# Performance work log

Hardware: AMD Instinct MI355X
Metric: run time of the kernel (lower is better)

## Reference

```python
import jax, jax.numpy as jnp
import numpy as np
import math

N_HEADS = 16  # from init_kwargs

def setup_inputs() -> dict:
    key = jax.random.key(0)
    ks = jax.random.split(key, 8)
    B, S, D = 2, 2048, 1024
    dk = D // N_HEADS
    # rotary frequencies: theta_i = 10000^(-2i/dk), angles = pos * theta
    inv_freq = 1.0 / (10000.0 ** (jnp.arange(0, dk, 2, dtype=jnp.float32) / dk))
    angles = jnp.arange(S, dtype=jnp.float32)[:, None] * inv_freq[None, :]  # [S, dk/2]
    scale = 0.02
    return {
        "x": jax.random.normal(ks[0], (B, S, D), dtype=jnp.float32),
        "freq_cos": jnp.cos(angles),
        "freq_sin": jnp.sin(angles),
        "Wq": jax.random.normal(ks[1], (D, D), dtype=jnp.float32) * scale,
        "Wk": jax.random.normal(ks[2], (D, D), dtype=jnp.float32) * scale,
        "Wv": jax.random.normal(ks[3], (D, D), dtype=jnp.float32) * scale,
        "Wo": jax.random.normal(ks[4], (D, D), dtype=jnp.float32) * scale,
    }

def _apply_rope(t, freq_cos, freq_sin):
    # t: [B, S, H, dk]; interpret last dim as dk/2 complex pairs (even=real, odd=imag)
    B, S, H, dk = t.shape
    tr = t.reshape(B, S, H, dk // 2, 2)
    re, im = tr[..., 0], tr[..., 1]
    c = freq_cos[None, :, None, :]  # [1, S, 1, dk/2]
    s = freq_sin[None, :, None, :]
    out_re = re * c - im * s
    out_im = re * s + im * c
    return jnp.stack([out_re, out_im], axis=-1).reshape(B, S, H, dk)

def reference(x, freq_cos, freq_sin, Wq, Wk, Wv, Wo):
    B, S, D = x.shape
    H = N_HEADS
    dk = D // H
    q = (x @ Wq).reshape(B, S, H, dk)
    k = (x @ Wk).reshape(B, S, H, dk)
    v = (x @ Wv).reshape(B, S, H, dk)
    q = _apply_rope(q, freq_cos, freq_sin)
    k = _apply_rope(k, freq_cos, freq_sin)
    # [B, H, S, dk]
    q = q.transpose(0, 2, 1, 3)
    k = k.transpose(0, 2, 1, 3)
    v = v.transpose(0, 2, 1, 3)
    scores = jnp.einsum('bhqd,bhkd->bhqk', q, k) / math.sqrt(dk)
    # faithful to source: softmax applied TWICE
    p = jax.nn.softmax(scores, axis=-1)
    p = jax.nn.softmax(p, axis=-1)
    out = jnp.einsum('bhqk,bhkd->bhqd', p, v)
    out = out.transpose(0, 2, 1, 3).reshape(B, S, D)
    return out @ Wo
```

## Files before the change

kernel.cpp:

```cpp
#include <hip/hip_runtime.h>
#include <cstdint>

typedef unsigned short u16;
typedef unsigned int u32;
typedef __attribute__((ext_vector_type(8))) short bf16x8;
typedef __attribute__((ext_vector_type(4))) short bf16x4;
typedef __attribute__((ext_vector_type(4))) float f32x4;

__device__ __forceinline__ float bf2f(short h) {
  union { u32 u; float f; } x; x.u = ((u32)(u16)h) << 16; return x.f;
}
__device__ __forceinline__ short f2bf(float f) {
  union { float f; u32 u; } x; x.f = f;
  u32 r = x.u + 0x7fffu + ((x.u >> 16) & 1u);
  return (short)(u16)(r >> 16);
}

__device__ __forceinline__ void gload16(const void* g, void* l) {
  __builtin_amdgcn_global_load_lds(
      (const __attribute__((address_space(1))) u32*)g,
      (__attribute__((address_space(3))) u32*)l, 16, 0, 0);
}

__global__ __launch_bounds__(256) void cast_k(const float* __restrict__ in,
                                              u16* __restrict__ out) {
  int i = blockIdx.x * 256 + threadIdx.x;
  const float4* p = (const float4*)(in + (size_t)i * 8);
  float4 a = p[0], b = p[1];
  bf16x8 v;
  v[0] = f2bf(a.x); v[1] = f2bf(a.y); v[2] = f2bf(a.z); v[3] = f2bf(a.w);
  v[4] = f2bf(b.x); v[5] = f2bf(b.y); v[6] = f2bf(b.z); v[7] = f2bf(b.w);
  *(bf16x8*)(out + (size_t)i * 8) = v;
}

__global__ __launch_bounds__(256) void castT4_k(
    const float* __restrict__ W0, const float* __restrict__ W1,
    const float* __restrict__ W2, const float* __restrict__ W3,
    u16* __restrict__ O0, u16* __restrict__ O1,
    u16* __restrict__ O2, u16* __restrict__ O3) {
  __shared__ u16 Ts[64 * 72];
  const int z = blockIdx.z;
  const float* in = z == 0 ? W0 : (z == 1 ? W1 : (z == 2 ? W2 : W3));
  u16* out = z == 0 ? O0 : (z == 1 ? O1 : (z == 2 ? O2 : O3));
  const int k0 = blockIdx.x * 64, n0 = blockIdx.y * 64;
  const int t = threadIdx.x;
  const int kr = t >> 4, nc = (t & 15) * 4;
#pragma unroll
  for (int p = 0; p < 4; ++p) {
    float4 v = *(const float4*)(in + (size_t)(k0 + kr + p * 16) * 1024 + n0 + nc);
    int kk = kr + p * 16;
    Ts[(nc + 0) * 72 + kk] = (u16)f2bf(v.x);
    Ts[(nc + 1) * 72 + kk] = (u16)f2bf(v.y);
    Ts[(nc + 2) * 72 + kk] = (u16)f2bf(v.z);
    Ts[(nc + 3) * 72 + kk] = (u16)f2bf(v.w);
  }
  __syncthreads();
  const int nr = t >> 2, kc = (t & 3) * 16;
  bf16x8 o0, o1;
#pragma unroll
  for (int j = 0; j < 8; ++j) {
    o0[j] = (short)Ts[nr * 72 + kc + j];
    o1[j] = (short)Ts[nr * 72 + kc + 8 + j];
  }
  *(bf16x8*)(out + (size_t)(n0 + nr) * 1024 + k0 + kc) = o0;
  *(bf16x8*)(out + (size_t)(n0 + nr) * 1024 + k0 + kc + 8) = o1;
}

template <int OUT_BF16, int NJ>
__device__ __forceinline__ void gemm_body(char* gsm, const u16* __restrict__ A,
                                          const u16* __restrict__ Bt,
                                          void* __restrict__ Cv,
                                          int row0, int col0) {
  constexpr int SB = 16384 + NJ * 4096;
  const int t = threadIdx.x;
  const int l = t & 63, w = t >> 6;
  const int lq = l & 15, g = l >> 4;
  const int wr = w >> 1, wc = w & 1;
  const int r8 = t >> 3;
  const int c8 = (((t & 7) ^ (r8 & 7)) << 3);

  f32x4 acc[4][NJ] = {};

  auto stage = [&](int cb, int k0) {
    char* dst = gsm + cb * SB + w * 1024;
#pragma unroll
    for (int p = 0; p < 4; ++p)
      gload16(A + (size_t)(row0 + r8 + 32 * p) * 1024 + k0 + c8, dst + p * 4096);
#pragma unroll
    for (int p = 0; p < NJ; ++p)
      gload16(Bt + (size_t)(col0 + r8 + 32 * p) * 1024 + k0 + c8,
              dst + 16384 + p * 4096);
  };

  stage(0, 0);
  __syncthreads();
  int cur = 0;
  for (int k0 = 0; k0 < 1024; k0 += 64) {
    if (k0 + 64 < 1024) stage(cur ^ 1, k0 + 64);
    const char* Ab = gsm + cur * SB;
#pragma unroll
    for (int ks = 0; ks < 2; ++ks) {
      bf16x8 af[4], bfr[NJ];
      const int sA = ks * 4 + g;
#pragma unroll
      for (int i = 0; i < 4; ++i) {
        int ra = wr * 64 + i * 16 + lq;
        af[i] = *(const bf16x8*)(Ab + ra * 128 + ((sA ^ (ra & 7)) << 4));
      }
#pragma unroll
      for (int j = 0; j < NJ; ++j) {
        int rb = wc * (NJ * 16) + j * 16 + lq;
        bfr[j] = *(const bf16x8*)(Ab + 16384 + rb * 128 + ((sA ^ (rb & 7)) << 4));
      }
#pragma unroll
      for (int i = 0; i < 4; ++i)
#pragma unroll
        for (int j = 0; j < NJ; ++j)
          acc[i][j] = __builtin_amdgcn_mfma_f32_16x16x32_bf16(af[i], bfr[j],
                                                              acc[i][j], 0, 0, 0);
    }
    __syncthreads();
    cur ^= 1;
  }

#pragma unroll
  for (int i = 0; i < 4; ++i)
#pragma unroll
    for (int j = 0; j < NJ; ++j)
#pragma unroll
      for (int jr = 0; jr < 4; ++jr) {
        int row = row0 + wr * 64 + i * 16 + 4 * g + jr;
        int col = col0 + wc * (NJ * 16) + j * 16 + lq;
        float v = acc[i][j][jr];
        if (OUT_BF16)
          ((u16*)Cv)[(size_t)row * 1024 + col] = (u16)f2bf(v);
        else
          ((float*)Cv)[(size_t)row * 1024 + col] = v;
      }
}

__global__ __launch_bounds__(256) void gemm_qkv_k(
    const u16* __restrict__ xb, const u16* __restrict__ Wqt,
    const u16* __restrict__ Wkt, const u16* __restrict__ Wvt,
    u16* __restrict__ Qr, u16* __restrict__ Kr, u16* __restrict__ Vr) {
  __shared__ __align__(16) char gsm[65536];
  const int which = blockIdx.y >> 3;
  const u16* Bt = which == 0 ? Wqt : (which == 1 ? Wkt : Wvt);
  u16* C = which == 0 ? Qr : (which == 1 ? Kr : Vr);
  gemm_body<1, 4>(gsm, xb, Bt, (void*)C, blockIdx.x * 128, (blockIdx.y & 7) * 128);
}

__global__ __launch_bounds__(256) void gemm_o_k(const u16* __restrict__ A,
                                                const u16* __restrict__ Bt,
                                                float* __restrict__ C) {
  __shared__ __align__(16) char gsm[49152];
  gemm_body<0, 2>(gsm, A, Bt, (void*)C, blockIdx.x * 128, blockIdx.y * 64);
}

__global__ __launch_bounds__(256) void rope2_k(const u16* __restrict__ Qr,
                                               const u16* __restrict__ Kr,
                                               u16* __restrict__ Qb,
                                               u16* __restrict__ Kb,
                                               const float* __restrict__ cosT,
                                               const float* __restrict__ sinT) {
  const int z = blockIdx.y;
  const u16* in = z ? Kr : Qr;
  u16* out = z ? Kb : Qb;
  const float scale = z ? 1.0f : 0.18033688011112042f;
  int i = blockIdx.x * 256 + threadIdx.x;
  size_t e = (size_t)i * 8;
  int m = (int)(e >> 10), n = (int)(e & 1023);
  int b = m >> 11, s = m & 2047, h = n >> 6, d = n & 63;
  float4 c4 = *(const float4*)(cosT + s * 32 + (d >> 1));
  float4 s4 = *(const float4*)(sinT + s * 32 + (d >> 1));
  bf16x8 v = *(const bf16x8*)(in + e);
  float cc[4] = {c4.x, c4.y, c4.z, c4.w}, sn[4] = {s4.x, s4.y, s4.z, s4.w};
  bf16x8 o;
#pragma unroll
  for (int j = 0; j < 4; ++j) {
    float re = bf2f(v[2 * j]), im = bf2f(v[2 * j + 1]);
    o[2 * j] = f2bf((re * cc[j] - im * sn[j]) * scale);
    o[2 * j + 1] = f2bf((re * sn[j] + im * cc[j]) * scale);
  }
  *(bf16x8*)(out + ((size_t)((b * 16 + h) * 2048 + s)) * 64 + d) = o;
}

__global__ __launch_bounds__(256) void transV_k(const u16* __restrict__ Vr,
                                                u16* __restrict__ Vt) {
  __shared__ u16 Ls[64 * 72];
  const int bh = blockIdx.y, s0 = blockIdx.x * 64;
  const int b = bh >> 4, h = bh & 15;
  const int t = threadIdx.x;
  const int sr = t >> 3, su = t & 7;
#pragma unroll
  for (int p = 0; p < 2; ++p) {
    int srow = sr + p * 32;
    bf16x8 v = *(const bf16x8*)(Vr + (size_t)(b * 2048 + s0 + srow) * 1024 + h * 64 + su * 8);
    *(bf16x8*)((char*)Ls + (srow * 72 + su * 8) * 2) = v;
  }
  __syncthreads();
  const int d = t >> 2, sc = (t & 3) * 16;
  const int base = (sc & 32) + ((sc >> 4) & 1) * 4;
  u16* dst = Vt + ((size_t)bh * 64 + d) * 2048 + s0 + base;
#pragma unroll
  for (int q = 0; q < 4; ++q) {
    bf16x4 c;
#pragma unroll
    for (int jj = 0; jj < 4; ++jj) c[jj] = (short)Ls[(sc + q * 4 + jj) * 72 + d];
    *(bf16x4*)(dst + 8 * q) = c;
  }
}

__global__ __launch_bounds__(256) void sumv_k(const u16* __restrict__ Vr,
                                              float* __restrict__ sumVp) {
  __shared__ float Ls[32][64];
  const int h = blockIdx.x, b = blockIdx.y, sl = blockIdx.z;
  const int t = threadIdx.x;
  const int d0 = (t & 7) * 8, rg = t >> 3;
  float a[8] = {};
#pragma unroll 4
  for (int i = 0; i < 16; ++i) {
    int r = sl * 512 + rg + i * 32;
    bf16x8 v = *(const bf16x8*)(Vr + (size_t)(b * 2048 + r) * 1024 + h * 64 + d0);
#pragma unroll
    for (int j = 0; j < 8; ++j) a[j] += bf2f(v[j]);
  }
#pragma unroll
  for (int j = 0; j < 8; ++j) Ls[rg][d0 + j] = a[j];
  __syncthreads();
  if (t < 64) {
    float tot = 0.f;
#pragma unroll
    for (int r2 = 0; r2 < 32; ++r2) tot += Ls[r2][t];
    sumVp[((size_t)sl * 32 + b * 16 + h) * 64 + t] = tot;
  }
}

__global__ __launch_bounds__(256) void attn_k(const u16* __restrict__ Qb,
                                              const u16* __restrict__ Kb,
                                              const u16* __restrict__ Vt,
                                              const float* __restrict__ sumVp,
                                              u16* __restrict__ Cb) {
  __shared__ __align__(16) char smem[33280];
  float* Lbuf = (float*)(smem + 32768);
  const int t = threadIdx.x;
  const int l = t & 63, w = t >> 6;
  const int lq = l & 15, g = l >> 4;
  const int qh = w & 1, kh = w >> 1;
  const int bh = blockIdx.y, q0 = blockIdx.x * 32;
  const int b = bh >> 4, h = bh & 15;

  const u16* qrow = Qb + ((size_t)bh * 2048 + q0 + qh * 16 + lq) * 64;
  const bf16x8 qf0 = *(const bf16x8*)(qrow + g * 8);
  const bf16x8 qf1 = *(const bf16x8*)(qrow + 32 + g * 8);

  const int r8 = t >> 3;
  const int c8 = (((t & 7) ^ (r8 & 7)) << 3);
  const size_t kbase = (size_t)bh * 2048 * 64;
  const size_t vbase = (size_t)bh * 64 * 2048;

  auto stage = [&](int cb, int j0) {
    char* dst = smem + cb * 16384 + w * 1024;
#pragma unroll
    for (int p = 0; p < 2; ++p) {
      gload16(Kb + kbase + (size_t)(j0 + r8 + 32 * p) * 64 + c8, dst + p * 4096);
      gload16(Vt + vbase + (size_t)(r8 + 32 * p) * 2048 + j0 + c8,
              dst + 8192 + p * 4096);
    }
  };

  float l1 = 0.0f;
  f32x4 accO[4] = {};

  stage(0, 0);
  __syncthreads();
  int cur = 0;
  for (int j0 = 0; j0 < 2048; j0 += 64) {
    if (j0 + 64 < 2048) stage(cur ^ 1, j0 + 64);
    const char* Kl = smem + cur * 16384;
    const char* Vl = Kl + 8192;
    f32x4 sc[2] = {};
#pragma unroll
    for (int ks = 0; ks < 2; ++ks)
#pragma unroll
      for (int kt = 0; kt < 2; ++kt) {
        int r = kh * 32 + kt * 16 + lq, sA = ks * 4 + g;
        bf16x8 af = *(const bf16x8*)(Kl + r * 128 + ((sA ^ (r & 7)) << 4));
        sc[kt] = __builtin_amdgcn_mfma_f32_16x16x32_bf16(af, ks ? qf1 : qf0,
                                                         sc[kt], 0, 0, 0);
      }
    float wv[2][4];
#pragma unroll
    for (int kt = 0; kt < 2; ++kt)
#pragma unroll
      for (int jr = 0; jr < 4; ++jr) {
        float e;
        asm("v_exp_f32 %0, %1" : "=v"(e) : "v"(sc[kt][jr]));
        wv[kt][jr] = e;
        l1 += e;
      }
    union { bf16x8 v; u32 uw[4]; } pb;
    asm("v_cvt_pk_bf16_f32 %0, %1, %2" : "=v"(pb.uw[0]) : "v"(wv[0][0]), "v"(wv[0][1]));
    asm("v_cvt_pk_bf16_f32 %0, %1, %2" : "=v"(pb.uw[1]) : "v"(wv[0][2]), "v"(wv[0][3]));
    asm("v_cvt_pk_bf16_f32 %0, %1, %2" : "=v"(pb.uw[2]) : "v"(wv[1][0]), "v"(wv[1][1]));
    asm("v_cvt_pk_bf16_f32 %0, %1, %2" : "=v"(pb.uw[3]) : "v"(wv[1][2]), "v"(wv[1][3]));
#pragma unroll
    for (int dt = 0; dt < 4; ++dt) {
      int dd = dt * 16 + lq;
      bf16x8 av = *(const bf16x8*)(Vl + dd * 128 +
                                   (((kh * 4 + g) ^ (dd & 7)) << 4));
      accO[dt] = __builtin_amdgcn_mfma_f32_16x16x32_bf16(av, pb.v, accO[dt], 0, 0, 0);
    }
    __syncthreads();
    cur ^= 1;
  }

  l1 += __shfl_xor(l1, 16);
  l1 += __shfl_xor(l1, 32);
  if (l < 16) Lbuf[w * 16 + l] = l1;
  __syncthreads();
  const float l1tot = Lbuf[w * 16 + lq] + Lbuf[(w ^ 2) * 16 + lq];
  const float rl1 = 1.0f / l1tot;

  float* Tb = (float*)smem;
  if (kh == 0) {
#pragma unroll
    for (int dt = 0; dt < 4; ++dt)
#pragma unroll
      for (int jr = 0; jr < 4; ++jr)
        Tb[(qh * 16 + lq) * 65 + dt * 16 + 4 * g + jr] = accO[dt][jr];
    if (l < 16) Lbuf[64 + qh * 16 + l] = rl1;
  }
  __syncthreads();
  if (kh == 1) {
#pragma unroll
    for (int dt = 0; dt < 4; ++dt)
#pragma unroll
      for (int jr = 0; jr < 4; ++jr)
        Tb[(qh * 16 + lq) * 65 + dt * 16 + 4 * g + jr] += accO[dt][jr];
  }
  __syncthreads();
  const int qq = t >> 3, dc = (t & 7) * 8;
  const float rq = Lbuf[64 + qq];
  f32x4 s0 = {}, s1 = {};
#pragma unroll
  for (int sl = 0; sl < 4; ++sl) {
    s0 += *(const f32x4*)(sumVp + ((size_t)sl * 32 + bh) * 64 + dc);
    s1 += *(const f32x4*)(sumVp + ((size_t)sl * 32 + bh) * 64 + dc + 4);
  }
  const float inv2049 = 1.0f / 2049.0f;
  bf16x8 o;
#pragma unroll
  for (int j = 0; j < 4; ++j) {
    o[j]     = f2bf((Tb[qq * 65 + dc + j] * rq + s0[j]) * inv2049);
    o[4 + j] = f2bf((Tb[qq * 65 + dc + 4 + j] * rq + s1[j]) * inv2049);
  }
  size_t obase = ((size_t)(b * 2048 + q0 + qq)) * 1024 + h * 64 + dc;
  *(bf16x8*)(Cb + obase) = o;
}

extern "C" void kernel_launch(void* const* d_in, const int* in_sizes, int n_in,
                              void* d_out, int out_size, void* d_ws, size_t ws_size,
                              hipStream_t stream) {
  const float* x = (const float*)d_in[0];
  const float* fcos = (const float*)d_in[1];
  const float* fsin = (const float*)d_in[2];
  const float* Wq = (const float*)d_in[3];
  const float* Wk = (const float*)d_in[4];
  const float* Wv = (const float*)d_in[5];
  const float* Wo = (const float*)d_in[6];
  float* out = (float*)d_out;

  char* wsp = (char*)d_ws;
  u16* xb  = (u16*)(wsp);
  u16* Wqt = (u16*)(wsp + (8ull << 20));
  u16* Wkt = (u16*)(wsp + (10ull << 20));
  u16* Wvt = (u16*)(wsp + (12ull << 20));
  u16* Wot = (u16*)(wsp + (14ull << 20));
  u16* Qr  = (u16*)(wsp + (16ull << 20));
  u16* Kr  = (u16*)(wsp + (24ull << 20));
  u16* Vr  = (u16*)(wsp + (32ull << 20));
  u16* Qb  = (u16*)(wsp + (40ull << 20));
  u16* Kb  = (u16*)(wsp + (48ull << 20));
  u16* Vt  = (u16*)(wsp + (56ull << 20));
  float* sumVp = (float*)(wsp + (8ull << 20));
  u16* Cb  = Qr;

  cast_k<<<2048, 256, 0, stream>>>(x, xb);
  dim3 gT(16, 16, 4);
  castT4_k<<<gT, 256, 0, stream>>>(Wq, Wk, Wv, Wo, Wqt, Wkt, Wvt, Wot);

  dim3 gQKV(32, 24);
  gemm_qkv_k<<<gQKV, 256, 0, stream>>>(xb, Wqt, Wkt, Wvt, Qr, Kr, Vr);

  dim3 gR(2048, 2);
  rope2_k<<<gR, 256, 0, stream>>>(Qr, Kr, Qb, Kb, fcos, fsin);
  dim3 gV(32, 32);
  transV_k<<<gV, 256, 0, stream>>>(Vr, Vt);
  dim3 gS(16, 2, 4);
  sumv_k<<<gS, 256, 0, stream>>>(Vr, sumVp);

  dim3 gA(64, 32);
  attn_k<<<gA, 256, 0, stream>>>(Qb, Kb, Vt, sumVp, Cb);

  dim3 gO(32, 16);
  gemm_o_k<<<gO, 256, 0, stream>>>(Cb, Wot, out);
}
```

Baseline: 202.7 us.

## Fuse Q rope into attention, fold V sum into transpose, use vmcnt-based pipelining

Q rotary embedding and scaling now happen inside the attention kernel when Q fragments are loaded, so the separate Q rope pass and its intermediate buffer go away. The V column-sum is computed inside the V transpose kernel as 32 per-block partials, removing the sumv kernel. The attention reduction now reads 32 partials instead of 4. The GEMM and attention loops replace __syncthreads with explicit vmcnt waits plus raw barriers, so the next stage's loads stay in flight while the current tile is computed. This removes two launches and one full pass over Q, but the hand-set wait counts are fragile.

```diff
diff --git a/kernel.cpp b/kernel.cpp
--- a/kernel.cpp
+++ b/kernel.cpp
@@ -21,6 +21,10 @@
       (const __attribute__((address_space(1))) u32*)g,
       (__attribute__((address_space(3))) u32*)l, 16, 0, 0);
 }
+
+#define WAITV(N) asm volatile("s_waitcnt vmcnt(" #N ")" ::: "memory")
+#define BARRIER() do { asm volatile("" ::: "memory"); \
+  __builtin_amdgcn_s_barrier(); asm volatile("" ::: "memory"); } while (0)
 
 __global__ __launch_bounds__(256) void cast_k(const float* __restrict__ in,
                                               u16* __restrict__ out) {
@@ -93,10 +97,16 @@
   };
 
   stage(0, 0);
-  __syncthreads();
   int cur = 0;
   for (int k0 = 0; k0 < 1024; k0 += 64) {
-    if (k0 + 64 < 1024) stage(cur ^ 1, k0 + 64);
+    if (k0 + 64 < 1024) {
+      stage(cur ^ 1, k0 + 64);
+      if constexpr (NJ == 4) WAITV(8); else WAITV(6);
+    } else {
+      WAITV(0);
+    }
+    BARRIER();
+    __builtin_amdgcn_sched_barrier(0);
     const char* Ab = gsm + cur * SB;
 #pragma unroll
     for (int ks = 0; ks < 2; ++ks) {
@@ -119,7 +129,7 @@
           acc[i][j] = __builtin_amdgcn_mfma_f32_16x16x32_bf16(af[i], bfr[j],
                                                               acc[i][j], 0, 0, 0);
     }
-    __syncthreads();
+    BARRIER();
     cur ^= 1;
   }
 
@@ -157,37 +167,33 @@
   gemm_body<0, 2>(gsm, A, Bt, (void*)C, blockIdx.x * 128, blockIdx.y * 64);
 }
 
-__global__ __launch_bounds__(256) void rope2_k(const u16* __restrict__ Qr,
-                                               const u16* __restrict__ Kr,
-                                               u16* __restrict__ Qb,
+__global__ __launch_bounds__(256) void ropeK_k(const u16* __restrict__ Kr,
                                                u16* __restrict__ Kb,
                                                const float* __restrict__ cosT,
                                                const float* __restrict__ sinT) {
-  const int z = blockIdx.y;
-  const u16* in = z ? Kr : Qr;
-  u16* out = z ? Kb : Qb;
-  const float scale = z ? 1.0f : 0.18033688011112042f;
   int i = blockIdx.x * 256 + threadIdx.x;
   size_t e = (size_t)i * 8;
   int m = (int)(e >> 10), n = (int)(e & 1023);
   int b = m >> 11, s = m & 2047, h = n >> 6, d = n & 63;
   float4 c4 = *(const float4*)(cosT + s * 32 + (d >> 1));
   float4 s4 = *(const float4*)(sinT + s * 32 + (d >> 1));
-  bf16x8 v = *(const bf16x8*)(in + e);
+  bf16x8 v = *(const bf16x8*)(Kr + e);
   float cc[4] = {c4.x, c4.y, c4.z, c4.w}, sn[4] = {s4.x, s4.y, s4.z, s4.w};
   bf16x8 o;
 #pragma unroll
   for (int j = 0; j < 4; ++j) {
     float re = bf2f(v[2 * j]), im = bf2f(v[2 * j + 1]);
-    o[2 * j] = f2bf((re * cc[j] - im * sn[j]) * scale);
-    o[2 * j + 1] = f2bf((re * sn[j] + im * cc[j]) * scale);
-  }
-  *(bf16x8*)(out + ((size_t)((b * 16 + h) * 2048 + s)) * 64 + d) = o;
+    o[2 * j] = f2bf(re * cc[j] - im * sn[j]);
+    o[2 * j + 1] = f2bf(re * sn[j] + im * cc[j]);
+  }
+  *(bf16x8*)(Kb + ((size_t)((b * 16 + h) * 2048 + s)) * 64 + d) = o;
 }
 
 __global__ __launch_bounds__(256) void transV_k(const u16* __restrict__ Vr,
-                                                u16* __restrict__ Vt) {
+                                                u16* __restrict__ Vt,
+                                                float* __restrict__ sumVp) {
   __shared__ u16 Ls[64 * 72];
+  __shared__ float Sbuf[4][64];
   const int bh = blockIdx.y, s0 = blockIdx.x * 64;
   const int b = bh >> 4, h = bh & 15;
   const int t = threadIdx.x;
@@ -209,37 +215,23 @@
     for (int jj = 0; jj < 4; ++jj) c[jj] = (short)Ls[(sc + q * 4 + jj) * 72 + d];
     *(bf16x4*)(dst + 8 * q) = c;
   }
-}
-
-__global__ __launch_bounds__(256) void sumv_k(const u16* __restrict__ Vr,
-                                              float* __restrict__ sumVp) {
-  __shared__ float Ls[32][64];
-  const int h = blockIdx.x, b = blockIdx.y, sl = blockIdx.z;
-  const int t = threadIdx.x;
-  const int d0 = (t & 7) * 8, rg = t >> 3;
-  float a[8] = {};
-#pragma unroll 4
-  for (int i = 0; i < 16; ++i) {
-    int r = sl * 512 + rg + i * 32;
-    bf16x8 v = *(const bf16x8*)(Vr + (size_t)(b * 2048 + r) * 1024 + h * 64 + d0);
-#pragma unroll
-    for (int j = 0; j < 8; ++j) a[j] += bf2f(v[j]);
-  }
-#pragma unroll
-  for (int j = 0; j < 8; ++j) Ls[rg][d0 + j] = a[j];
-  __syncthreads();
-  if (t < 64) {
-    float tot = 0.f;
-#pragma unroll
-    for (int r2 = 0; r2 < 32; ++r2) tot += Ls[r2][t];
-    sumVp[((size_t)sl * 32 + b * 16 + h) * 64 + t] = tot;
-  }
-}
-
-__global__ __launch_bounds__(256) void attn_k(const u16* __restrict__ Qb,
+  const int d2 = t & 63, seg = t >> 6;
+  float part = 0.f;
+#pragma unroll
+  for (int rr = 0; rr < 16; ++rr) part += bf2f((short)Ls[(seg * 16 + rr) * 72 + d2]);
+  Sbuf[seg][d2] = part;
+  __syncthreads();
+  if (t < 64)
+    sumVp[((size_t)blockIdx.x * 32 + bh) * 64 + t] =
+        Sbuf[0][t] + Sbuf[1][t] + Sbuf[2][t] + Sbuf[3][t];
+}
+
+__global__ __launch_bounds__(256) void attn_k(const u16* __restrict__ Qr,
                                               const u16* __restrict__ Kb,
                                               const u16* __restrict__ Vt,
                                               const float* __restrict__ sumVp,
+                                              const float* __restrict__ cosT,
+                                              const float* __restrict__ sinT,
                                               u16* __restrict__ Cb) {
   __shared__ __align__(16) char smem[33280];
   float* Lbuf = (float*)(smem + 32768);
@@ -250,9 +242,27 @@
   const int bh = blockIdx.y, q0 = blockIdx.x * 32;
   const int b = bh >> 4, h = bh & 15;
 
-  const u16* qrow = Qb + ((size_t)bh * 2048 + q0 + qh * 16 + lq) * 64;
-  const bf16x8 qf0 = *(const bf16x8*)(qrow + g * 8);
-  const bf16x8 qf1 = *(const bf16x8*)(qrow + 32 + g * 8);
+  const int sQ = q0 + qh * 16 + lq;
+  const u16* qr = Qr + (size_t)(b * 2048 + sQ) * 1024 + h * 64;
+  bf16x8 r0 = *(const bf16x8*)(qr + g * 8);
+  bf16x8 r1 = *(const bf16x8*)(qr + 32 + g * 8);
+  float4 c0 = *(const float4*)(cosT + sQ * 32 + g * 4);
+  float4 n0 = *(const float4*)(sinT + sQ * 32 + g * 4);
+  float4 c1 = *(const float4*)(cosT + sQ * 32 + 16 + g * 4);
+  float4 n1 = *(const float4*)(sinT + sQ * 32 + 16 + g * 4);
+  const float SC = 0.18033688011112042f;
+  float cc0[4] = {c0.x, c0.y, c0.z, c0.w}, ss0[4] = {n0.x, n0.y, n0.z, n0.w};
+  float cc1[4] = {c1.x, c1.y, c1.z, c1.w}, ss1[4] = {n1.x, n1.y, n1.z, n1.w};
+  bf16x8 qf0, qf1;
+#pragma unroll
+  for (int j = 0; j < 4; ++j) {
+    float re = bf2f(r0[2 * j]), im = bf2f(r0[2 * j + 1]);
+    qf0[2 * j]     = f2bf((re * cc0[j] - im * ss0[j]) * SC);
+    qf0[2 * j + 1] = f2bf((re * ss0[j] + im * cc0[j]) * SC);
+    re = bf2f(r1[2 * j]); im = bf2f(r1[2 * j + 1]);
+    qf1[2 * j]     = f2bf((re * cc1[j] - im * ss1[j]) * SC);
+    qf1[2 * j + 1] = f2bf((re * ss1[j] + im * cc1[j]) * SC);
+  }
 
   const int r8 = t >> 3;
   const int c8 = (((t & 7) ^ (r8 & 7)) << 3);
@@ -273,10 +283,16 @@
   f32x4 accO[4] = {};
 
   stage(0, 0);
-  __syncthreads();
   int cur = 0;
   for (int j0 = 0; j0 < 2048; j0 += 64) {
-    if (j0 + 64 < 2048) stage(cur ^ 1, j0 + 64);
+    if (j0 + 64 < 2048) {
+      stage(cur ^ 1, j0 + 64);
+      WAITV(4);
+    } else {
+      WAITV(0);
+    }
+    BARRIER();
+    __builtin_amdgcn_sched_barrier(0);
     const char* Kl = smem + cur * 16384;
     const char* Vl = Kl + 8192;
     f32x4 sc[2] = {};
@@ -311,7 +327,7 @@
                                    (((kh * 4 + g) ^ (dd & 7)) << 4));
       accO[dt] = __builtin_amdgcn_mfma_f32_16x16x32_bf16(av, pb.v, accO[dt], 0, 0, 0);
     }
-    __syncthreads();
+    BARRIER();
     cur ^= 1;
   }
 
@@ -343,8 +359,8 @@
   const int qq = t >> 3, dc = (t & 7) * 8;
   const float rq = Lbuf[64 + qq];
   f32x4 s0 = {}, s1 = {};
-#pragma unroll
-  for (int sl = 0; sl < 4; ++sl) {
+#pragma unroll 8
+  for (int sl = 0; sl < 32; ++sl) {
     s0 += *(const f32x4*)(sumVp + ((size_t)sl * 32 + bh) * 64 + dc);
     s1 += *(const f32x4*)(sumVp + ((size_t)sl * 32 + bh) * 64 + dc + 4);
   }
@@ -380,7 +396,6 @@
   u16* Qr  = (u16*)(wsp + (16ull << 20));
   u16* Kr  = (u16*)(wsp + (24ull << 20));
   u16* Vr  = (u16*)(wsp + (32ull << 20));
-  u16* Qb  = (u16*)(wsp + (40ull << 20));
   u16* Kb  = (u16*)(wsp + (48ull << 20));
   u16* Vt  = (u16*)(wsp + (56ull << 20));
   float* sumVp = (float*)(wsp + (8ull << 20));
@@ -393,15 +408,12 @@
   dim3 gQKV(32, 24);
   gemm_qkv_k<<<gQKV, 256, 0, stream>>>(xb, Wqt, Wkt, Wvt, Qr, Kr, Vr);
 
-  dim3 gR(2048, 2);
-  rope2_k<<<gR, 256, 0, stream>>>(Qr, Kr, Qb, Kb, fcos, fsin);
+  ropeK_k<<<2048, 256, 0, stream>>>(Kr, Kb, fcos, fsin);
   dim3 gV(32, 32);
-  transV_k<<<gV, 256, 0, stream>>>(Vr, Vt);
-  dim3 gS(16, 2, 4);
-  sumv_k<<<gS, 256, 0, stream>>>(Vr, sumVp);
+  transV_k<<<gV, 256, 0, stream>>>(Vr, Vt, sumVp);
 
   dim3 gA(64, 32);
-  attn_k<<<gA, 256, 0, stream>>>(Qb, Kb, Vt, sumVp, Cb);
+  attn_k<<<gA, 256, 0, stream>>>(Qr, Kb, Vt, sumVp, fcos, fsin, Cb);
 
   dim3 gO(32, 16);
   gemm_o_k<<<gO, 256, 0, stream>>>(Cb, Wot, out);
```

Measured after the change: 211.9 us. 1.05x slower.

## Fuse RoPE into QKV GEMM epilogue and V column sums into transpose

Applied to the files above, without the earlier changes.

The QKV GEMM epilogue now applies rotary embedding and the query scale directly, using a lane shuffle to fetch each pair partner, and writes Q/K in head-major layout. This removes the separate RoPE kernel and its round trip through global memory. The V transpose kernel also produces per-tile column sums, which replaces the sumv kernel, and the attention kernel sums 32 partials instead of 4. Attention blocks are remapped with an XCD-aware swizzle. The cost is scattered 2-byte stores and per-element cos/sin loads in the GEMM epilogue.

```diff
diff --git a/kernel.cpp b/kernel.cpp
--- a/kernel.cpp
+++ b/kernel.cpp
@@ -66,11 +66,11 @@
   *(bf16x8*)(out + (size_t)(n0 + nr) * 1024 + k0 + kc + 8) = o1;
 }
 
-template <int OUT_BF16, int NJ>
-__device__ __forceinline__ void gemm_body(char* gsm, const u16* __restrict__ A,
+template <int NJ>
+__device__ __forceinline__ void gemm_core(char* gsm, const u16* __restrict__ A,
                                           const u16* __restrict__ Bt,
-                                          void* __restrict__ Cv,
-                                          int row0, int col0) {
+                                          int row0, int col0,
+                                          f32x4 (&acc)[4][NJ]) {
   constexpr int SB = 16384 + NJ * 4096;
   const int t = threadIdx.x;
   const int l = t & 63, w = t >> 6;
@@ -78,8 +78,6 @@
   const int wr = w >> 1, wc = w & 1;
   const int r8 = t >> 3;
   const int c8 = (((t & 7) ^ (r8 & 7)) << 3);
-
-  f32x4 acc[4][NJ] = {};
 
   auto stage = [&](int cb, int k0) {
     char* dst = gsm + cb * SB + w * 1024;
@@ -122,72 +120,89 @@
     __syncthreads();
     cur ^= 1;
   }
-
-#pragma unroll
-  for (int i = 0; i < 4; ++i)
-#pragma unroll
-    for (int j = 0; j < NJ; ++j)
-#pragma unroll
-      for (int jr = 0; jr < 4; ++jr) {
-        int row = row0 + wr * 64 + i * 16 + 4 * g + jr;
-        int col = col0 + wc * (NJ * 16) + j * 16 + lq;
-        float v = acc[i][j][jr];
-        if (OUT_BF16)
-          ((u16*)Cv)[(size_t)row * 1024 + col] = (u16)f2bf(v);
-        else
-          ((float*)Cv)[(size_t)row * 1024 + col] = v;
-      }
 }
 
 __global__ __launch_bounds__(256) void gemm_qkv_k(
     const u16* __restrict__ xb, const u16* __restrict__ Wqt,
     const u16* __restrict__ Wkt, const u16* __restrict__ Wvt,
-    u16* __restrict__ Qr, u16* __restrict__ Kr, u16* __restrict__ Vr) {
+    u16* __restrict__ Qb, u16* __restrict__ Kb, u16* __restrict__ Vr,
+    const float* __restrict__ cosT, const float* __restrict__ sinT) {
   __shared__ __align__(16) char gsm[65536];
   const int which = blockIdx.y >> 3;
   const u16* Bt = which == 0 ? Wqt : (which == 1 ? Wkt : Wvt);
-  u16* C = which == 0 ? Qr : (which == 1 ? Kr : Vr);
-  gemm_body<1, 4>(gsm, xb, Bt, (void*)C, blockIdx.x * 128, (blockIdx.y & 7) * 128);
+  const int row0 = blockIdx.x * 128, col0 = (blockIdx.y & 7) * 128;
+
+  f32x4 acc[4][4] = {};
+  gemm_core<4>(gsm, xb, Bt, row0, col0, acc);
+
+  const int t = threadIdx.x;
+  const int l = t & 63, w = t >> 6;
+  const int lq = l & 15, g = l >> 4;
+  const int wr = w >> 1, wc = w & 1;
+  const float SC = 0.18033688011112042f;
+
+  if (which == 2) {
+#pragma unroll
+    for (int i = 0; i < 4; ++i)
+#pragma unroll
+      for (int j = 0; j < 4; ++j)
+#pragma unroll
+        for (int jr = 0; jr < 4; ++jr) {
+          int row = row0 + wr * 64 + i * 16 + 4 * g + jr;
+          int col = col0 + wc * 64 + j * 16 + lq;
+          Vr[(size_t)row * 1024 + col] = (u16)f2bf(acc[i][j][jr]);
+        }
+  } else {
+    u16* dstB = which == 0 ? Qb : Kb;
+    const float sc = which == 0 ? SC : 1.0f;
+#pragma unroll
+    for (int i = 0; i < 4; ++i)
+#pragma unroll
+      for (int j = 0; j < 4; ++j)
+#pragma unroll
+        for (int jr = 0; jr < 4; ++jr) {
+          int row = row0 + wr * 64 + i * 16 + 4 * g + jr;
+          int col = col0 + wc * 64 + j * 16 + lq;
+          int bb = row >> 11, ss = row & 2047;
+          int hh = col >> 6, dd = col & 63;
+          float v = acc[i][j][jr];
+          float pv = __shfl_xor(v, 1);
+          float c = cosT[ss * 32 + (dd >> 1)];
+          float s = sinT[ss * 32 + (dd >> 1)];
+          float o = (dd & 1) ? (pv * s + v * c) : (v * c - pv * s);
+          dstB[(((size_t)bb * 16 + hh) * 2048 + ss) * 64 + dd] = (u16)f2bf(o * sc);
+        }
+  }
 }
 
 __global__ __launch_bounds__(256) void gemm_o_k(const u16* __restrict__ A,
                                                 const u16* __restrict__ Bt,
                                                 float* __restrict__ C) {
   __shared__ __align__(16) char gsm[49152];
-  gemm_body<0, 2>(gsm, A, Bt, (void*)C, blockIdx.x * 128, blockIdx.y * 64);
-}
-
-__global__ __launch_bounds__(256) void rope2_k(const u16* __restrict__ Qr,
-                                               const u16* __restrict__ Kr,
-                                               u16* __restrict__ Qb,
-                                               u16* __restrict__ Kb,
-                                               const float* __restrict__ cosT,
-                                               const float* __restrict__ sinT) {
-  const int z = blockIdx.y;
-  const u16* in = z ? Kr : Qr;
-  u16* out = z ? Kb : Qb;
-  const float scale = z ? 1.0f : 0.18033688011112042f;
-  int i = blockIdx.x * 256 + threadIdx.x;
-  size_t e = (size_t)i * 8;
-  int m = (int)(e >> 10), n = (int)(e & 1023);
-  int b = m >> 11, s = m & 2047, h = n >> 6, d = n & 63;
-  float4 c4 = *(const float4*)(cosT + s * 32 + (d >> 1));
-  float4 s4 = *(const float4*)(sinT + s * 32 + (d >> 1));
-  bf16x8 v = *(const bf16x8*)(in + e);
-  float cc[4] = {c4.x, c4.y, c4.z, c4.w}, sn[4] = {s4.x, s4.y, s4.z, s4.w};
-  bf16x8 o;
-#pragma unroll
-  for (int j = 0; j < 4; ++j) {
-    float re = bf2f(v[2 * j]), im = bf2f(v[2 * j + 1]);
-    o[2 * j] = f2bf((re * cc[j] - im * sn[j]) * scale);
-    o[2 * j + 1] = f2bf((re * sn[j] + im * cc[j]) * scale);
-  }
-  *(bf16x8*)(out + ((size_t)((b * 16 + h) * 2048 + s)) * 64 + d) = o;
+  const int row0 = blockIdx.x * 128, col0 = blockIdx.y * 64;
+  f32x4 acc[4][2] = {};
+  gemm_core<2>(gsm, A, Bt, row0, col0, acc);
+  const int t = threadIdx.x;
+  const int l = t & 63, w = t >> 6;
+  const int lq = l & 15, g = l >> 4;
+  const int wr = w >> 1, wc = w & 1;
+#pragma unroll
+  for (int i = 0; i < 4; ++i)
+#pragma unroll
+    for (int j = 0; j < 2; ++j)
+#pragma unroll
+      for (int jr = 0; jr < 4; ++jr) {
+        int row = row0 + wr * 64 + i * 16 + 4 * g + jr;
+        int col = col0 + wc * 32 + j * 16 + lq;
+        C[(size_t)row * 1024 + col] = acc[i][j][jr];
+      }
 }
 
 __global__ __launch_bounds__(256) void transV_k(const u16* __restrict__ Vr,
-                                                u16* __restrict__ Vt) {
+                                                u16* __restrict__ Vt,
+                                                float* __restrict__ sumVp) {
   __shared__ u16 Ls[64 * 72];
+  __shared__ float Sbuf[4][64];
   const int bh = blockIdx.y, s0 = blockIdx.x * 64;
   const int b = bh >> 4, h = bh & 15;
   const int t = threadIdx.x;
@@ -209,31 +224,15 @@
     for (int jj = 0; jj < 4; ++jj) c[jj] = (short)Ls[(sc + q * 4 + jj) * 72 + d];
     *(bf16x4*)(dst + 8 * q) = c;
   }
-}
-
-__global__ __launch_bounds__(256) void sumv_k(const u16* __restrict__ Vr,
-                                              float* __restrict__ sumVp) {
-  __shared__ float Ls[32][64];
-  const int h = blockIdx.x, b = blockIdx.y, sl = blockIdx.z;
-  const int t = threadIdx.x;
-  const int d0 = (t & 7) * 8, rg = t >> 3;
-  float a[8] = {};
-#pragma unroll 4
-  for (int i = 0; i < 16; ++i) {
-    int r = sl * 512 + rg + i * 32;
-    bf16x8 v = *(const bf16x8*)(Vr + (size_t)(b * 2048 + r) * 1024 + h * 64 + d0);
-#pragma unroll
-    for (int j = 0; j < 8; ++j) a[j] += bf2f(v[j]);
-  }
-#pragma unroll
-  for (int j = 0; j < 8; ++j) Ls[rg][d0 + j] = a[j];
-  __syncthreads();
-  if (t < 64) {
-    float tot = 0.f;
-#pragma unroll
-    for (int r2 = 0; r2 < 32; ++r2) tot += Ls[r2][t];
-    sumVp[((size_t)sl * 32 + b * 16 + h) * 64 + t] = tot;
-  }
+  const int d2 = t & 63, seg = t >> 6;
+  float part = 0.f;
+#pragma unroll
+  for (int rr = 0; rr < 16; ++rr) part += bf2f((short)Ls[(seg * 16 + rr) * 72 + d2]);
+  Sbuf[seg][d2] = part;
+  __syncthreads();
+  if (t < 64)
+    sumVp[((size_t)blockIdx.x * 32 + bh) * 64 + t] =
+        Sbuf[0][t] + Sbuf[1][t] + Sbuf[2][t] + Sbuf[3][t];
 }
 
 __global__ __launch_bounds__(256) void attn_k(const u16* __restrict__ Qb,
@@ -247,12 +246,15 @@
   const int l = t & 63, w = t >> 6;
   const int lq = l & 15, g = l >> 4;
   const int qh = w & 1, kh = w >> 1;
-  const int bh = blockIdx.y, q0 = blockIdx.x * 32;
+  const int bid = blockIdx.y * 64 + blockIdx.x;
+  const int wg = (bid & 7) * 256 + (bid >> 3);
+  const int bh = wg >> 6, q0 = (wg & 63) * 32;
   const int b = bh >> 4, h = bh & 15;
 
-  const u16* qrow = Qb + ((size_t)bh * 2048 + q0 + qh * 16 + lq) * 64;
-  const bf16x8 qf0 = *(const bf16x8*)(qrow + g * 8);
-  const bf16x8 qf1 = *(const bf16x8*)(qrow + 32 + g * 8);
+  const int sQ = q0 + qh * 16 + lq;
+  const u16* qr = Qb + ((size_t)bh * 2048 + sQ) * 64;
+  const bf16x8 qf0 = *(const bf16x8*)(qr + g * 8);
+  const bf16x8 qf1 = *(const bf16x8*)(qr + 32 + g * 8);
 
   const int r8 = t >> 3;
   const int c8 = (((t & 7) ^ (r8 & 7)) << 3);
@@ -343,8 +345,8 @@
   const int qq = t >> 3, dc = (t & 7) * 8;
   const float rq = Lbuf[64 + qq];
   f32x4 s0 = {}, s1 = {};
-#pragma unroll
-  for (int sl = 0; sl < 4; ++sl) {
+#pragma unroll 8
+  for (int sl = 0; sl < 32; ++sl) {
     s0 += *(const f32x4*)(sumVp + ((size_t)sl * 32 + bh) * 64 + dc);
     s1 += *(const f32x4*)(sumVp + ((size_t)sl * 32 + bh) * 64 + dc + 4);
   }
@@ -377,28 +379,23 @@
   u16* Wkt = (u16*)(wsp + (10ull << 20));
   u16* Wvt = (u16*)(wsp + (12ull << 20));
   u16* Wot = (u16*)(wsp + (14ull << 20));
-  u16* Qr  = (u16*)(wsp + (16ull << 20));
-  u16* Kr  = (u16*)(wsp + (24ull << 20));
+  u16* Qb  = (u16*)(wsp + (16ull << 20));
+  u16* Kb  = (u16*)(wsp + (24ull << 20));
   u16* Vr  = (u16*)(wsp + (32ull << 20));
-  u16* Qb  = (u16*)(wsp + (40ull << 20));
-  u16* Kb  = (u16*)(wsp + (48ull << 20));
-  u16* Vt  = (u16*)(wsp + (56ull << 20));
+  u16* Vt  = (u16*)(wsp + (40ull << 20));
+  u16* Cb  = (u16*)(wsp + (48ull << 20));
   float* sumVp = (float*)(wsp + (8ull << 20));
-  u16* Cb  = Qr;
 
   cast_k<<<2048, 256, 0, stream>>>(x, xb);
   dim3 gT(16, 16, 4);
   castT4_k<<<gT, 256, 0, stream>>>(Wq, Wk, Wv, Wo, Wqt, Wkt, Wvt, Wot);
 
   dim3 gQKV(32, 24);
-  gemm_qkv_k<<<gQKV, 256, 0, stream>>>(xb, Wqt, Wkt, Wvt, Qr, Kr, Vr);
-
-  dim3 gR(2048, 2);
-  rope2_k<<<gR, 256, 0, stream>>>(Qr, Kr, Qb, Kb, fcos, fsin);
+  gemm_qkv_k<<<gQKV, 256, 0, stream>>>(xb, Wqt, Wkt, Wvt, Qb, Kb, Vr,
+                                       fcos, fsin);
+
   dim3 gV(32, 32);
-  transV_k<<<gV, 256, 0, stream>>>(Vr, Vt);
-  dim3 gS(16, 2, 4);
-  sumv_k<<<gS, 256, 0, stream>>>(Vr, sumVp);
+  transV_k<<<gV, 256, 0, stream>>>(Vr, Vt, sumVp);
 
   dim3 gA(64, 32);
   attn_k<<<gA, 256, 0, stream>>>(Qb, Kb, Vt, sumVp, Cb);
```

New measurement: 208.1 us. 2.6% more time.
